# Performance work log

Measured on AMD Instinct MI355X. Metric: run time of the kernel, lower is better.

## Reference

```python
import jax, jax.numpy as jnp
import numpy as np

N_CLASSES = 2  # FS-MOL binary labels


def setup_inputs() -> dict:
    key = jax.random.key(0)
    k1, k2, k3 = jax.random.split(key, 3)
    Ns, Nq, d = 512, 16384, 512
    support_features = jax.random.normal(k1, (Ns, d), dtype=jnp.float32)
    support_labels = jax.random.randint(k2, (Ns,), 0, N_CLASSES, dtype=jnp.int64)
    query_features = jax.random.normal(k3, (Nq, d), dtype=jnp.float32)
    return {
        "support_features": support_features,
        "support_labels": support_labels,
        "query_features": query_features,
    }


def _cov(x):
    # rowvar=False covariance of [N, d] -> [d, d], matching _estimate_cov
    xc = x - jnp.mean(x, axis=0, keepdims=True)
    return (xc.T @ xc) / (x.shape[0] - 1)


def reference(support_features, support_labels, query_features):
    d = support_features.shape[1]
    dt = support_features.dtype
    task_cov = _cov(support_features)          # [d, d]
    reg = jnp.asarray(0.1, dt) * jnp.eye(d, dtype=dt)

    def per_class(c):
        mask = (support_labels == c).astype(dt)            # [Ns]
        n = mask.sum()                                      # scalar count
        mean = (mask[:, None] * support_features).sum(0) / n
        xc = (support_features - mean) * mask[:, None]      # zero out other classes
        cov_c = (xc.T @ xc) / (n - 1.0)
        lam = jnp.minimum(n / (n + 1.0), jnp.asarray(0.1, dt))
        prec = jnp.linalg.inv(lam * cov_c + (1.0 - lam) * task_cov + reg)
        return mean, prec

    means, precs = jax.vmap(per_class)(jnp.arange(N_CLASSES))  # [C,d], [C,d,d]

    # Mahalanobis: diff[c,q,:] = mean_c - query_q  (matches repeated_class_means - repeated_target)
    diff = means[:, None, :] - query_features[None, :, :]      # [C, Nq, d]
    h = jnp.einsum('cqd,cde->cqe', diff, precs)                # [C, Nq, d]
    logits = -(h * diff).sum(-1).T                             # [Nq, C]
    return logits
```

## Files before the change

### kernel.cpp

```cpp
#include <hip/hip_runtime.h>

#define NS 512
#define DF 512
#define NQ 16384

#define WS_MEAN0 0
#define WS_MEAN1 512
#define WS_MEANA 1024
#define WS_CNT   1536
#define WS_V0    2048
#define WS_V1    2560
#define WS_KC    3072
#define WS_M     4096
#define WS_PB    (WS_M + 2*DF*DF)
#define WS_QB    (WS_PB + DF*DF)
#define WS_GP    WS_QB
#define WS_UC    WS_PB
#define WS_VC    (WS_PB + 2*2*8*4096)

typedef __attribute__((ext_vector_type(8))) short short8;
typedef __attribute__((ext_vector_type(4))) float floatx4;

__device__ __forceinline__ unsigned short f2bf(float f) {
    unsigned u = __float_as_uint(f);
    unsigned r = (u + 0x7fffu + ((u >> 16) & 1u)) >> 16;
    return (unsigned short)r;
}

__device__ __forceinline__ float readlane_f(float v, int lane) {
    return __uint_as_float(__builtin_amdgcn_readlane(__float_as_uint(v), lane));
}

__device__ __forceinline__ void load_lds16(const void* g, void* l) {
    __builtin_amdgcn_global_load_lds(
        (const __attribute__((address_space(1))) unsigned int*)g,
        (__attribute__((address_space(3))) unsigned int*)l, 16, 0, 0);
}

__device__ __forceinline__ void gj_invert64(float* T, float (*rbuf)[4][64], int tid) {
    int jl = tid & 63, w = tid >> 6;
    float Tr[16];
#pragma unroll
    for (int m = 0; m < 16; ++m) Tr[m] = T[(w * 16 + m) * 66 + jl];
#pragma unroll
    for (int r = 0; r < 16; ++r) {
        const int q0 = r * 4;
        const int par = r & 1;
        if (w == (q0 >> 4)) {
            const int mb = q0 & 15;
            rbuf[par][0][jl] = Tr[mb + 0];
            rbuf[par][1][jl] = Tr[mb + 1];
            rbuf[par][2][jl] = Tr[mb + 2];
            rbuf[par][3][jl] = Tr[mb + 3];
        }
        __syncthreads();
        float B[4][4];
#pragma unroll
        for (int a = 0; a < 4; ++a)
#pragma unroll
            for (int bb = 0; bb < 4; ++bb) B[a][bb] = rbuf[par][a][q0 + bb];
#pragma unroll
        for (int p = 0; p < 4; ++p) {
            float piv = 1.0f / B[p][p];
#pragma unroll
            for (int j = 0; j < 4; ++j) if (j != p) B[p][j] *= piv;
#pragma unroll
            for (int i = 0; i < 4; ++i) if (i != p) {
                float f = B[i][p];
#pragma unroll
                for (int j = 0; j < 4; ++j) if (j != p) B[i][j] -= f * B[p][j];
                B[i][p] = -f * piv;
            }
            B[p][p] = piv;
        }
        float r0v = rbuf[par][0][jl], r1v = rbuf[par][1][jl];
        float r2v = rbuf[par][2][jl], r3v = rbuf[par][3][jl];
        float nr[4];
#pragma unroll
        for (int a = 0; a < 4; ++a)
            nr[a] = B[a][0] * r0v + B[a][1] * r1v + B[a][2] * r2v + B[a][3] * r3v;
        bool colin = ((jl >> 2) == r);
        int bsel = jl & 3;
        float Bc[4];
#pragma unroll
        for (int a = 0; a < 4; ++a)
            Bc[a] = bsel == 0 ? B[a][0]
                  : (bsel == 1 ? B[a][1] : (bsel == 2 ? B[a][2] : B[a][3]));
#pragma unroll
        for (int m = 0; m < 16; ++m) {
            float cv0 = readlane_f(Tr[m], q0 + 0);
            float cv1 = readlane_f(Tr[m], q0 + 1);
            float cv2 = readlane_f(Tr[m], q0 + 2);
            float cv3 = readlane_f(Tr[m], q0 + 3);
            float g = Tr[m] - (cv0 * nr[0] + cv1 * nr[1] + cv2 * nr[2] + cv3 * nr[3]);
            bool rowin = (((w * 16 + m) >> 2) == r);
            float gcol = -(cv0 * Bc[0] + cv1 * Bc[1] + cv2 * Bc[2] + cv3 * Bc[3]);
            if (rowin) g = nr[m & 3];
            if (colin) g = rowin ? Bc[m & 3] : gcol;
            Tr[m] = g;
        }
    }
#pragma unroll
    for (int m = 0; m < 16; ++m) T[(w * 16 + m) * 66 + jl] = Tr[m];
    __syncthreads();
}

__global__ __launch_bounds__(256) void k_front(const float* __restrict__ S,
                                               const int* __restrict__ lab,
                                               float* __restrict__ ws) {
    int b = blockIdx.x, tid = threadIdx.x;
    if (b >= 512) {
        __shared__ int slb[NS];
        __shared__ float r0[4][64], r1[4][64];
        __shared__ int rc[4];
        int bs = b - 512;
        for (int l = tid; l < NS; l += 256) slb[l] = lab[l];
        __syncthreads();
        int dl = tid & 63, ch = tid >> 6;
        int dd = bs * 64 + dl;
        float s0 = 0.f, s1 = 0.f;
        int n1 = 0;
        for (int n = ch * 128; n < ch * 128 + 128; ++n) {
            float v = S[n * DF + dd];
            if (slb[n]) { s1 += v; n1++; } else { s0 += v; }
        }
        r0[ch][dl] = s0; r1[ch][dl] = s1;
        if (dl == 0) rc[ch] = n1;
        __syncthreads();
        if (ch == 0) {
            float t0 = 0.f, t1 = 0.f; int n1t = 0;
#pragma unroll
            for (int x = 0; x < 4; ++x) { t0 += r0[x][dl]; t1 += r1[x][dl]; n1t += rc[x]; }
            float fn1 = (float)n1t, fn0 = (float)(NS - n1t);
            ws[WS_MEAN0 + dd] = t0 / fn0;
            ws[WS_MEAN1 + dd] = t1 / fn1;
            ws[WS_MEANA + dd] = (t0 + t1) / (float)NS;
            if (bs == 0 && dl == 0) {
                ws[WS_CNT] = fn0; ws[WS_CNT + 1] = fn1;
                ws[WS_KC] = 0.f; ws[WS_KC + 1] = 0.f;
            }
        }
        return;
    }
    __shared__ float SA[16 * 65];
    __shared__ float SB[16 * 65];
    __shared__ int lb[16];
    int tx = tid & 15, ty = tid >> 4;
    int i0 = (b & 7) * 64, j0 = ((b >> 3) & 7) * 64;
    int z = b >> 6;
    float a0[4][4] = {{0.f}}, a1[4][4] = {{0.f}};
    for (int nc = z * 64; nc < z * 64 + 64; nc += 16) {
#pragma unroll
        for (int l = 0; l < 4; ++l) {
            int idx = tid + 256 * l;
            int nn = idx >> 6, col = idx & 63;
            SA[nn * 65 + col] = S[(nc + nn) * DF + i0 + col];
            SB[nn * 65 + col] = S[(nc + nn) * DF + j0 + col];
        }
        if (tid < 16) lb[tid] = lab[nc + tid];
        __syncthreads();
#pragma unroll
        for (int kk = 0; kk < 16; ++kk) {
            float av[4], bv[4];
#pragma unroll
            for (int r = 0; r < 4; ++r) av[r] = SA[kk * 65 + ty * 4 + r];
#pragma unroll
            for (int s = 0; s < 4; ++s) bv[s] = SB[kk * 65 + tx * 4 + s];
            if (lb[kk]) {
#pragma unroll
                for (int r = 0; r < 4; ++r)
#pragma unroll
                    for (int s = 0; s < 4; ++s) a1[r][s] += av[r] * bv[s];
            } else {
#pragma unroll
                for (int r = 0; r < 4; ++r)
#pragma unroll
                    for (int s = 0; s < 4; ++s) a0[r][s] += av[r] * bv[s];
            }
        }
        __syncthreads();
    }
    float* Gp = ws + WS_GP;
#pragma unroll
    for (int r = 0; r < 4; ++r) {
        int i = i0 + ty * 4 + r;
#pragma unroll
        for (int s = 0; s < 4; ++s) {
            int j = j0 + tx * 4 + s;
            Gp[((z * 2 + 0) * DF + i) * DF + j] = a0[r][s];
            Gp[((z * 2 + 1) * DF + i) * DF + j] = a1[r][s];
        }
    }
}

__global__ __launch_bounds__(256) void k_asm(float* __restrict__ ws) {
    int b = blockIdx.x, tid = threadIdx.x;
    int tx = tid & 15, ty = tid >> 4;
    __shared__ float T[64 * 66];
    __shared__ float rbuf[2][4][64];
    const float* Gp = ws + WS_GP;
    float n0 = ws[WS_CNT], n1 = ws[WS_CNT + 1];
    float lam0 = fminf(n0 / (n0 + 1.f), 0.1f);
    float lam1 = fminf(n1 / (n1 + 1.f), 0.1f);
    bool dup = (b == 64);
    int ti = dup ? 0 : (b >> 3), tj = dup ? 0 : (b & 7);
    int jb = tj * 64 + tx * 4;
    float4 m0j = *(const float4*)&ws[WS_MEAN0 + jb];
    float4 m1j = *(const float4*)&ws[WS_MEAN1 + jb];
    float4 maj = *(const float4*)&ws[WS_MEANA + jb];
    float out0[4][4], out1[4][4];
#pragma unroll
    for (int r = 0; r < 4; ++r) {
        int i = ti * 64 + ty * 4 + r;
        float m0i = ws[WS_MEAN0 + i], m1i = ws[WS_MEAN1 + i], mai = ws[WS_MEANA + i];
        float4 g0 = make_float4(0.f, 0.f, 0.f, 0.f);
        float4 g1 = make_float4(0.f, 0.f, 0.f, 0.f);
#pragma unroll
        for (int ch = 0; ch < 8; ++ch) {
            float4 a = *(const float4*)&Gp[((ch * 2 + 0) * DF + i) * DF + jb];
            float4 bb = *(const float4*)&Gp[((ch * 2 + 1) * DF + i) * DF + jb];
            g0.x += a.x; g0.y += a.y; g0.z += a.z; g0.w += a.w;
            g1.x += bb.x; g1.y += bb.y; g1.z += bb.z; g1.w += bb.w;
        }
        float g0a[4] = {g0.x, g0.y, g0.z, g0.w};
        float g1a[4] = {g1.x, g1.y, g1.z, g1.w};
        float m0ja[4] = {m0j.x, m0j.y, m0j.z, m0j.w};
        float m1ja[4] = {m1j.x, m1j.y, m1j.z, m1j.w};
        float maja[4] = {maj.x, maj.y, maj.z, maj.w};
#pragma unroll
        for (int s = 0; s < 4; ++s) {
            int j = jb + s;
            float task = (g0a[s] + g1a[s] - (float)NS * mai * maja[s]) / (float)(NS - 1);
            float cov0 = (g0a[s] - n0 * m0i * m0ja[s]) / (n0 - 1.f);
            float cov1 = (g1a[s] - n1 * m1i * m1ja[s]) / (n1 - 1.f);
            float dg = (i == j) ? 0.1f : 0.f;
            out0[r][s] = lam0 * cov0 + (1.f - lam0) * task + dg;
            out1[r][s] = lam1 * cov1 + (1.f - lam1) * task + dg;
        }
    }
    if (!dup) {
#pragma unroll
        for (int r = 0; r < 4; ++r) {
            int i = ti * 64 + ty * 4 + r;
            *(float4*)&ws[WS_M + (size_t)i * DF + jb] = make_float4(out0[r][0], out0[r][1], out0[r][2], out0[r][3]);
            *(float4*)&ws[WS_M + DF * DF + (size_t)i * DF + jb] = make_float4(out1[r][0], out1[r][1], out1[r][2], out1[r][3]);
        }
        if (ti == 0 && tj != 0) {
            float* u0 = ws + WS_UC + ((0 * 2 + 0) * 8 + tj) * 4096;
            float* u1 = ws + WS_UC + ((0 * 2 + 1) * 8 + tj) * 4096;
#pragma unroll
            for (int r = 0; r < 4; ++r) {
                int il = ty * 4 + r, jl = tx * 4;
                *(float4*)&u0[il * 64 + jl] = make_float4(out0[r][0], out0[r][1], out0[r][2], out0[r][3]);
                *(float4*)&u1[il * 64 + jl] = make_float4(out1[r][0], out1[r][1], out1[r][2], out1[r][3]);
            }
        }
        if (tj == 0 && ti != 0) {
            float* v0 = ws + WS_VC + ((0 * 2 + 0) * 8 + ti) * 4096;
            float* v1 = ws + WS_VC + ((0 * 2 + 1) * 8 + ti) * 4096;
#pragma unroll
            for (int r = 0; r < 4; ++r) {
                int il = ty * 4 + r, jl = tx * 4;
                *(float4*)&v0[il * 64 + jl] = make_float4(out0[r][0], out0[r][1], out0[r][2], out0[r][3]);
                *(float4*)&v1[il * 64 + jl] = make_float4(out1[r][0], out1[r][1], out1[r][2], out1[r][3]);
            }
        }
    }
    if (b == 0 || dup) {
#pragma unroll
        for (int r = 0; r < 4; ++r)
#pragma unroll
            for (int s = 0; s < 4; ++s)
                T[(ty * 4 + r) * 66 + tx * 4 + s] = dup ? out1[r][s] : out0[r][s];
        __syncthreads();
        gj_invert64(T, rbuf, tid);
        float* scr = ws + WS_UC + ((0 * 2 + (dup ? 1 : 0)) * 8 + 0) * 4096;
#pragma unroll
        for (int m = 0; m < 16; ++m) {
            int idx = tid + 256 * m;
            int i = idx >> 6, j = idx & 63;
            scr[i * 64 + j] = T[i * 66 + j];
        }
    }
}

__global__ __launch_bounds__(256) void k_fgj(float* __restrict__ ws, int k) {
    int c = blockIdx.y, jh = blockIdx.z;
    int x = blockIdx.x;
    int ti = x >> 3, tj = x & 7;
    int par = k & 1, npar = par ^ 1;
    int tid = threadIdx.x;
    int cb0 = jh * 32;
    float* Mb = ws + WS_M + (size_t)c * DF * DF;
    const float* UCi = ws + WS_UC + (par * 2 + c) * 8 * 4096;
    const float* VCi = ws + WS_VC + (par * 2 + c) * 8 * 4096;
    float* UCo = ws + WS_UC + (npar * 2 + c) * 8 * 4096;
    float* VCo = ws + WS_VC + (npar * 2 + c) * 8 * 4096;
    const float* scr_in = UCi + k * 4096;

    if (ti == k && tj == k) {
        float* Akk = Mb + (k * 64) * DF + k * 64;
#pragma unroll
        for (int m = 0; m < 8; ++m) {
            int idx = tid + 256 * m;
            int i = idx >> 5, j = idx & 31;
            Akk[i * DF + cb0 + j] = scr_in[i * 64 + cb0 + j];
        }
        return;
    }
    bool isrow = (ti == k);
    bool iscol = (tj == k);
    bool spec = (ti == k + 1) && (tj == k + 1);
    if ((iscol || spec) && jh == 1) return;

    __shared__ float T[64 * 68];
    __shared__ float V[64 * 66];
    __shared__ float U[64 * 68];
    __shared__ float D[64 * 68];
    __shared__ float rbuf[2][4][64];

#pragma unroll
    for (int m = 0; m < 16; ++m) {
        int idx = tid + 256 * m;
        int i = idx >> 6, j = idx & 63;
        T[i * 68 + j] = scr_in[i * 64 + j];
    }

    if (isrow) {
        const float* uc = UCi + tj * 4096;
#pragma unroll
        for (int m = 0; m < 8; ++m) {
            int idx = tid + 256 * m;
            int i = idx >> 5, j = idx & 31;
            U[i * 68 + j] = uc[i * 64 + cb0 + j];
        }
        __syncthreads();
        int tx8 = tid & 7, ty32 = tid >> 3;
        float acc[2][4] = {{0.f}};
#pragma unroll 8
        for (int kk = 0; kk < 64; ++kk) {
            float a0 = T[(ty32 * 2 + 0) * 68 + kk];
            float a1 = T[(ty32 * 2 + 1) * 68 + kk];
            float4 bv = *(const float4*)&U[kk * 68 + tx8 * 4];
            acc[0][0] += a0 * bv.x; acc[0][1] += a0 * bv.y; acc[0][2] += a0 * bv.z; acc[0][3] += a0 * bv.w;
            acc[1][0] += a1 * bv.x; acc[1][1] += a1 * bv.y; acc[1][2] += a1 * bv.z; acc[1][3] += a1 * bv.w;
        }
        float* dst = Mb + (k * 64) * DF + tj * 64 + cb0;
#pragma unroll
        for (int r = 0; r < 2; ++r) {
            int row = ty32 * 2 + r;
            float4 o = make_float4(acc[r][0], acc[r][1], acc[r][2], acc[r][3]);
            *(float4*)&dst[row * DF + tx8 * 4] = o;
            if (tj == k + 1)
                *(float4*)&VCo[k * 4096 + row * 64 + cb0 + tx8 * 4] = o;
        }
        return;
    }

    if (iscol) {
        const float* vc = VCi + ti * 4096;
#pragma unroll
        for (int m = 0; m < 16; ++m) {
            int idx = tid + 256 * m;
            int i = idx >> 6, j = idx & 63;
            V[i * 66 + j] = vc[i * 64 + j];
        }
        __syncthreads();
        int tx16 = tid & 15, ty16 = tid >> 4;
        float acc[4][4] = {{0.f}};
#pragma unroll 8
        for (int kk = 0; kk < 64; ++kk) {
            float a[4];
#pragma unroll
            for (int r = 0; r < 4; ++r) a[r] = V[(ty16 * 4 + r) * 66 + kk];
            float4 bv = *(const float4*)&T[kk * 68 + tx16 * 4];
#pragma unroll
            for (int r = 0; r < 4; ++r) {
                acc[r][0] += a[r] * bv.x; acc[r][1] += a[r] * bv.y;
                acc[r][2] += a[r] * bv.z; acc[r][3] += a[r] * bv.w;
            }
        }
        float* dst = Mb + (ti * 64) * DF + k * 64;
#pragma unroll
        for (int r = 0; r < 4; ++r) {
            int row = ty16 * 4 + r;
            float4 o = make_float4(-acc[r][0], -acc[r][1], -acc[r][2], -acc[r][3]);
            *(float4*)&dst[row * DF + tx16 * 4] = o;
            if (ti == k + 1)
                *(float4*)&UCo[k * 4096 + row * 64 + tx16 * 4] = o;
        }
        return;
    }

    if (!spec) {
        const float* vc = VCi + ti * 4096;
#pragma unroll
        for (int m = 0; m < 16; ++m) {
            int idx = tid + 256 * m;
            int i = idx >> 6, j = idx & 63;
            V[i * 66 + j] = vc[i * 64 + j];
        }
        const float* uc = UCi + tj * 4096;
#pragma unroll
        for (int m = 0; m < 8; ++m) {
            int idx = tid + 256 * m;
            int i = idx >> 5, j = idx & 31;
            U[i * 68 + j] = uc[i * 64 + cb0 + j];
        }
        __syncthreads();
        int tx8 = tid & 7, ty32 = tid >> 3;
        float a1[2][4] = {{0.f}};
#pragma unroll 8
        for (int kk = 0; kk < 64; ++kk) {
            float v0 = T[(ty32 * 2 + 0) * 68 + kk];
            float v1 = T[(ty32 * 2 + 1) * 68 + kk];
            float4 bv = *(const float4*)&U[kk * 68 + tx8 * 4];
            a1[0][0] += v0 * bv.x; a1[0][1] += v0 * bv.y; a1[0][2] += v0 * bv.z; a1[0][3] += v0 * bv.w;
            a1[1][0] += v1 * bv.x; a1[1][1] += v1 * bv.y; a1[1][2] += v1 * bv.z; a1[1][3] += v1 * bv.w;
        }
#pragma unroll
        for (int r = 0; r < 2; ++r)
            *(float4*)&D[(ty32 * 2 + r) * 68 + tx8 * 4] = make_float4(a1[r][0], a1[r][1], a1[r][2], a1[r][3]);
        __syncthreads();
        float a2[2][4] = {{0.f}};
#pragma unroll 8
        for (int kk = 0; kk < 64; ++kk) {
            float v0 = V[(ty32 * 2 + 0) * 66 + kk];
            float v1 = V[(ty32 * 2 + 1) * 66 + kk];
            float4 bv = *(const float4*)&D[kk * 68 + tx8 * 4];
            a2[0][0] += v0 * bv.x; a2[0][1] += v0 * bv.y; a2[0][2] += v0 * bv.z; a2[0][3] += v0 * bv.w;
            a2[1][0] += v1 * bv.x; a2[1][1] += v1 * bv.y; a2[1][2] += v1 * bv.z; a2[1][3] += v1 * bv.w;
        }
        float* dst = Mb + (ti * 64) * DF + tj * 64 + cb0;
#pragma unroll
        for (int r = 0; r < 2; ++r) {
            int row = ty32 * 2 + r;
            float4 old = *(const float4*)&dst[row * DF + tx8 * 4];
            float4 nv = make_float4(old.x - a2[r][0], old.y - a2[r][1], old.z - a2[r][2], old.w - a2[r][3]);
            *(float4*)&dst[row * DF + tx8 * 4] = nv;
            if (tj == k + 1)
                *(float4*)&VCo[ti * 4096 + row * 64 + cb0 + tx8 * 4] = nv;
            if (ti == k + 1)
                *(float4*)&UCo[tj * 4096 + row * 64 + cb0 + tx8 * 4] = nv;
        }
        return;
    }

    {
        const float* vc = VCi + (k + 1) * 4096;
#pragma unroll
        for (int m = 0; m < 16; ++m) {
            int idx = tid + 256 * m;
            int i = idx >> 6, j = idx & 63;
            V[i * 66 + j] = vc[i * 64 + j];
        }
        const float* uc = UCi + (k + 1) * 4096;
#pragma unroll
        for (int m = 0; m < 16; ++m) {
            int idx = tid + 256 * m;
            int i = idx >> 6, j = idx & 63;
            U[i * 68 + j] = uc[i * 64 + j];
        }
        __syncthreads();
        int tx16 = tid & 15, ty16 = tid >> 4;
        float d[4][4] = {{0.f}};
#pragma unroll 8
        for (int kk = 0; kk < 64; ++kk) {
            float a[4];
#pragma unroll
            for (int r = 0; r < 4; ++r) a[r] = T[(ty16 * 4 + r) * 68 + kk];
            float4 bv = *(const float4*)&U[kk * 68 + tx16 * 4];
#pragma unroll
            for (int r = 0; r < 4; ++r) {
                d[r][0] += a[r] * bv.x; d[r][1] += a[r] * bv.y;
                d[r][2] += a[r] * bv.z; d[r][3] += a[r] * bv.w;
            }
        }
#pragma unroll
        for (int r = 0; r < 4; ++r)
            *(float4*)&D[(ty16 * 4 + r) * 68 + tx16 * 4] = make_float4(d[r][0], d[r][1], d[r][2], d[r][3]);
        __syncthreads();
        float y[4][4] = {{0.f}};
#pragma unroll 8
        for (int kk = 0; kk < 64; ++kk) {
            float a[4];
#pragma unroll
            for (int r = 0; r < 4; ++r) a[r] = V[(ty16 * 4 + r) * 66 + kk];
            float4 bv = *(const float4*)&D[kk * 68 + tx16 * 4];
#pragma unroll
            for (int r = 0; r < 4; ++r) {
                y[r][0] += a[r] * bv.x; y[r][1] += a[r] * bv.y;
                y[r][2] += a[r] * bv.z; y[r][3] += a[r] * bv.w;
            }
        }
        const float* dst = Mb + (size_t)((k + 1) * 64) * DF + (k + 1) * 64;
        float4 nv[4];
#pragma unroll
        for (int r = 0; r < 4; ++r) {
            int row = ty16 * 4 + r;
            float4 old = *(const float4*)&dst[row * DF + tx16 * 4];
            nv[r] = make_float4(old.x - y[r][0], old.y - y[r][1], old.z - y[r][2], old.w - y[r][3]);
        }
        __syncthreads();
#pragma unroll
        for (int r = 0; r < 4; ++r) {
            int row = ty16 * 4 + r;
            V[row * 66 + tx16 * 4 + 0] = nv[r].x;
            V[row * 66 + tx16 * 4 + 1] = nv[r].y;
            V[row * 66 + tx16 * 4 + 2] = nv[r].z;
            V[row * 66 + tx16 * 4 + 3] = nv[r].w;
        }
        __syncthreads();
        gj_invert64(V, rbuf, tid);
        float* so = UCo + (k + 1) * 4096;
#pragma unroll
        for (int m = 0; m < 16; ++m) {
            int idx = tid + 256 * m;
            int i = idx >> 6, j = idx & 63;
            so[i * 64 + j] = V[i * 66 + j];
        }
    }
}

__global__ __launch_bounds__(256) void k_vkbf(float* __restrict__ ws) {
    int b = blockIdx.x;
    int tid = threadIdx.x;
    if (b >= 16) {
        int e = (b - 16) * 2048 + tid * 8;
        const float* M = ws + WS_M;
        unsigned short* pbw = (unsigned short*)(ws + WS_PB);
        float4 x0 = *(const float4*)&M[e];
        float4 x1 = *(const float4*)&M[e + 4];
        short8 r;
        r[0] = (short)f2bf(x0.x); r[1] = (short)f2bf(x0.y);
        r[2] = (short)f2bf(x0.z); r[3] = (short)f2bf(x0.w);
        r[4] = (short)f2bf(x1.x); r[5] = (short)f2bf(x1.y);
        r[6] = (short)f2bf(x1.z); r[7] = (short)f2bf(x1.w);
        *(short8*)(pbw + e) = r;
        return;
    }
    int c = b >> 3, rb = b & 7;
    const float* P = ws + WS_M + (size_t)c * DF * DF;
    const float* mc = ws + (c ? WS_MEAN1 : WS_MEAN0);
    float* v = ws + (c ? WS_V1 : WS_V0);
    __shared__ float ml[DF];
    __shared__ float red[4][64];
    for (int l = tid; l < DF; l += 256) ml[l] = mc[l];
    __syncthreads();
    int rl = tid & 63, ch = tid >> 6;
    int row = rb * 64 + rl;
    float dot = 0.f;
    const float* pr = P + (size_t)row * DF + ch * 128;
    for (int t = 0; t < 32; ++t) {
        float4 pv = *(const float4*)(pr + t * 4);
        const float* mm = ml + ch * 128 + t * 4;
        dot += pv.x * mm[0] + pv.y * mm[1] + pv.z * mm[2] + pv.w * mm[3];
    }
    red[ch][rl] = dot;
    __syncthreads();
    if (ch == 0) {
        float d = red[0][rl] + red[1][rl] + red[2][rl] + red[3][rl];
        v[row] = d;
        float kp = d * ml[row];
#pragma unroll
        for (int off = 32; off > 0; off >>= 1) kp += __shfl_down(kp, off);
        if (rl == 0) atomicAdd(&ws[WS_KC + c], kp);
    }
}

__global__ __launch_bounds__(256) void k_qinit(const float* __restrict__ Q,
                                               float* __restrict__ ws,
                                               float* __restrict__ out) {
    unsigned short* qbw = (unsigned short*)(ws + WS_QB);
    const float* v0 = ws + WS_V0;
    const float* v1 = ws + WS_V1;
    int lane = threadIdx.x & 63;
    int q = blockIdx.x * 4 + (threadIdx.x >> 6);
    const float* qrow = Q + (size_t)q * DF + lane * 8;
    float4 x0 = *(const float4*)(qrow);
    float4 x1 = *(const float4*)(qrow + 4);
    const float* v0p = v0 + lane * 8;
    const float* v1p = v1 + lane * 8;
    float4 w00 = *(const float4*)(v0p), w01 = *(const float4*)(v0p + 4);
    float4 w10 = *(const float4*)(v1p), w11 = *(const float4*)(v1p + 4);
    float a0 = x0.x * w00.x + x0.y * w00.y + x0.z * w00.z + x0.w * w00.w
             + x1.x * w01.x + x1.y * w01.y + x1.z * w01.z + x1.w * w01.w;
    float a1 = x0.x * w10.x + x0.y * w10.y + x0.z * w10.z + x0.w * w10.w
             + x1.x * w11.x + x1.y * w11.y + x1.z * w11.z + x1.w * w11.w;
    short8 r;
    r[0] = (short)f2bf(x0.x); r[1] = (short)f2bf(x0.y);
    r[2] = (short)f2bf(x0.z); r[3] = (short)f2bf(x0.w);
    r[4] = (short)f2bf(x1.x); r[5] = (short)f2bf(x1.y);
    r[6] = (short)f2bf(x1.z); r[7] = (short)f2bf(x1.w);
    *(short8*)(qbw + (size_t)q * DF + lane * 8) = r;
#pragma unroll
    for (int off = 32; off > 0; off >>= 1) {
        a0 += __shfl_down(a0, off);
        a1 += __shfl_down(a1, off);
    }
    if (lane == 0) {
        out[q * 2 + 0] = 2.f * a0 - ws[WS_KC + 0];
        out[q * 2 + 1] = 2.f * a1 - ws[WS_KC + 1];
    }
}

__global__ __launch_bounds__(256, 3) void k_gemm(const float* __restrict__ ws,
                                                 float* __restrict__ out) {
    const unsigned short* qb = (const unsigned short*)(ws + WS_QB);
    int c = blockIdx.y >> 2;
    int n0 = (blockIdx.y & 3) * 128;
    const unsigned short* pbc = (const unsigned short*)(ws + WS_PB) + (size_t)c * DF * DF;
    int q0 = blockIdx.x * 128;
    __shared__ __align__(16) unsigned short Abuf[128 * 64];
    __shared__ __align__(16) unsigned short Bbuf[128 * 64];
    int tid = threadIdx.x;
    int w = tid >> 6, lane = tid & 63;
    int quad = lane >> 4, l15 = lane & 15;
    floatx4 acc[2][8];
#pragma unroll
    for (int mt = 0; mt < 2; ++mt)
#pragma unroll
        for (int nt = 0; nt < 8; ++nt) acc[mt][nt] = (floatx4)(0.f);

    for (int kt = 0; kt < 8; ++kt) {
        int kc2 = kt * 64;
#pragma unroll
        for (int i = 0; i < 4; ++i) {
            int o = tid * 16 + i * 4096;
            int row = o >> 7;
            int sg = ((o >> 4) & 7) ^ (row & 7);
            load_lds16(qb + (size_t)(q0 + row) * DF + kc2 + sg * 8, (char*)Abuf + o);
        }
#pragma unroll
        for (int i = 0; i < 4; ++i) {
            int o = tid * 16 + i * 4096;
            int row = o >> 7;
            int sg = ((o >> 4) & 7) ^ (row & 7);
            load_lds16(pbc + (size_t)(n0 + row) * DF + kc2 + sg * 8, (char*)Bbuf + o);
        }
        __syncthreads();
#pragma unroll
        for (int kk2 = 0; kk2 < 2; ++kk2) {
            int u = ((kk2 * 4 + quad) ^ (l15 & 7)) << 4;
            short8 b[8];
#pragma unroll
            for (int nt = 0; nt < 8; ++nt)
                b[nt] = *(const short8*)((const char*)Bbuf + (nt * 16 + l15) * 128 + u);
#pragma unroll
            for (int mt = 0; mt < 2; ++mt) {
                short8 a = *(const short8*)((const char*)Abuf + (w * 32 + mt * 16 + l15) * 128 + u);
#pragma unroll
                for (int nt = 0; nt < 8; ++nt)
                    acc[mt][nt] = __builtin_amdgcn_mfma_f32_16x16x32_bf16(a, b[nt], acc[mt][nt], 0, 0, 0);
            }
        }
        __syncthreads();
    }
#pragma unroll
    for (int mt = 0; mt < 2; ++mt)
#pragma unroll
        for (int reg = 0; reg < 4; ++reg) {
            int row = w * 32 + mt * 16 + quad * 4 + reg;
            float part = 0.f;
#pragma unroll
            for (int nt = 0; nt < 8; ++nt) {
                float h = acc[mt][nt][reg];
                unsigned qu = qb[(size_t)(q0 + row) * DF + n0 + nt * 16 + l15];
                part += h * __uint_as_float(qu << 16);
            }
            part += __shfl_xor(part, 1);
            part += __shfl_xor(part, 2);
            part += __shfl_xor(part, 4);
            part += __shfl_xor(part, 8);
            if (l15 == 0) atomicAdd(&out[(size_t)(q0 + row) * 2 + c], -part);
        }
}

extern "C" void kernel_launch(void* const* d_in, const int* in_sizes, int n_in,
                              void* d_out, int out_size, void* d_ws, size_t ws_size,
                              hipStream_t stream) {
    const float* S = (const float*)d_in[0];
    const int* lab = (const int*)d_in[1];
    const float* Q = (const float*)d_in[2];
    float* out = (float*)d_out;
    float* ws = (float*)d_ws;

    k_front<<<520, 256, 0, stream>>>(S, lab, ws);
    k_asm<<<65, 256, 0, stream>>>(ws);
    for (int k = 0; k < 8; ++k)
        k_fgj<<<dim3(64, 2, 2), 256, 0, stream>>>(ws, k);
    k_vkbf<<<272, 256, 0, stream>>>(ws);
    k_qinit<<<NQ / 4, 256, 0, stream>>>(Q, ws, out);
    k_gemm<<<dim3(NQ / 128, 8), 256, 0, stream>>>(ws, out);
}
```

Baseline: 342.0 us.

## Overlap query bf16 conversion with the latency-bound block Gauss-Jordan launches

Adds extra blocks to each of the eight k_fgj launches that convert a slice of the query matrix from fp32 to bf16 into the workspace, filling otherwise idle GPU capacity. k_qinit then reads the bf16 copy instead of fp32 Q, so the later kernel does less memory traffic. The linear term now uses bf16-rounded queries, which slightly changes numerics. It also relies on the GP scratch that aliases the QB region not being used after these writes.

```diff
diff --git a/kernel.cpp b/kernel.cpp
--- a/kernel.cpp
+++ b/kernel.cpp
@@ -25,6 +25,10 @@
     unsigned u = __float_as_uint(f);
     unsigned r = (u + 0x7fffu + ((u >> 16) & 1u)) >> 16;
     return (unsigned short)r;
+}
+
+__device__ __forceinline__ float bf2f(unsigned short u) {
+    return __uint_as_float(((unsigned)u) << 16);
 }
 
 __device__ __forceinline__ float readlane_f(float v, int lane) {
@@ -284,12 +288,28 @@
     }
 }
 
-__global__ __launch_bounds__(256) void k_fgj(float* __restrict__ ws, int k) {
+__global__ __launch_bounds__(256) void k_fgj(const float* __restrict__ Q,
+                                             float* __restrict__ ws, int k) {
     int c = blockIdx.y, jh = blockIdx.z;
     int x = blockIdx.x;
+    int tid = threadIdx.x;
+
+    if (x >= 64) {
+        int cb = (x - 64) + 128 * (c + 2 * jh);
+        size_t e = (size_t)k * 1048576 + (size_t)cb * 2048 + tid * 8;
+        float4 x0 = *(const float4*)(Q + e);
+        float4 x1 = *(const float4*)(Q + e + 4);
+        short8 r;
+        r[0] = (short)f2bf(x0.x); r[1] = (short)f2bf(x0.y);
+        r[2] = (short)f2bf(x0.z); r[3] = (short)f2bf(x0.w);
+        r[4] = (short)f2bf(x1.x); r[5] = (short)f2bf(x1.y);
+        r[6] = (short)f2bf(x1.z); r[7] = (short)f2bf(x1.w);
+        *(short8*)((unsigned short*)(ws + WS_QB) + e) = r;
+        return;
+    }
+
     int ti = x >> 3, tj = x & 7;
     int par = k & 1, npar = par ^ 1;
-    int tid = threadIdx.x;
     int cb0 = jh * 32;
     float* Mb = ws + WS_M + (size_t)c * DF * DF;
     const float* UCi = ws + WS_UC + (par * 2 + c) * 8 * 4096;
@@ -568,31 +588,25 @@
     }
 }
 
-__global__ __launch_bounds__(256) void k_qinit(const float* __restrict__ Q,
-                                               float* __restrict__ ws,
+__global__ __launch_bounds__(256) void k_qinit(float* __restrict__ ws,
                                                float* __restrict__ out) {
-    unsigned short* qbw = (unsigned short*)(ws + WS_QB);
+    const unsigned short* qbw = (const unsigned short*)(ws + WS_QB);
     const float* v0 = ws + WS_V0;
     const float* v1 = ws + WS_V1;
     int lane = threadIdx.x & 63;
     int q = blockIdx.x * 4 + (threadIdx.x >> 6);
-    const float* qrow = Q + (size_t)q * DF + lane * 8;
-    float4 x0 = *(const float4*)(qrow);
-    float4 x1 = *(const float4*)(qrow + 4);
+    short8 qv = *(const short8*)(qbw + (size_t)q * DF + lane * 8);
+    float xx[8];
+#pragma unroll
+    for (int j = 0; j < 8; ++j) xx[j] = bf2f((unsigned short)qv[j]);
     const float* v0p = v0 + lane * 8;
     const float* v1p = v1 + lane * 8;
     float4 w00 = *(const float4*)(v0p), w01 = *(const float4*)(v0p + 4);
     float4 w10 = *(const float4*)(v1p), w11 = *(const float4*)(v1p + 4);
-    float a0 = x0.x * w00.x + x0.y * w00.y + x0.z * w00.z + x0.w * w00.w
-             + x1.x * w01.x + x1.y * w01.y + x1.z * w01.z + x1.w * w01.w;
-    float a1 = x0.x * w10.x + x0.y * w10.y + x0.z * w10.z + x0.w * w10.w
-             + x1.x * w11.x + x1.y * w11.y + x1.z * w11.z + x1.w * w11.w;
-    short8 r;
-    r[0] = (short)f2bf(x0.x); r[1] = (short)f2bf(x0.y);
-    r[2] = (short)f2bf(x0.z); r[3] = (short)f2bf(x0.w);
-    r[4] = (short)f2bf(x1.x); r[5] = (short)f2bf(x1.y);
-    r[6] = (short)f2bf(x1.z); r[7] = (short)f2bf(x1.w);
-    *(short8*)(qbw + (size_t)q * DF + lane * 8) = r;
+    float a0 = xx[0] * w00.x + xx[1] * w00.y + xx[2] * w00.z + xx[3] * w00.w
+             + xx[4] * w01.x + xx[5] * w01.y + xx[6] * w01.z + xx[7] * w01.w;
+    float a1 = xx[0] * w10.x + xx[1] * w10.y + xx[2] * w10.z + xx[3] * w10.w
+             + xx[4] * w11.x + xx[5] * w11.y + xx[6] * w11.z + xx[7] * w11.w;
 #pragma unroll
     for (int off = 32; off > 0; off >>= 1) {
         a0 += __shfl_down(a0, off);
@@ -688,8 +702,8 @@
     k_front<<<520, 256, 0, stream>>>(S, lab, ws);
     k_asm<<<65, 256, 0, stream>>>(ws);
     for (int k = 0; k < 8; ++k)
-        k_fgj<<<dim3(64, 2, 2), 256, 0, stream>>>(ws, k);
+        k_fgj<<<dim3(192, 2, 2), 256, 0, stream>>>(Q, ws, k);
     k_vkbf<<<272, 256, 0, stream>>>(ws);
-    k_qinit<<<NQ / 4, 256, 0, stream>>>(Q, ws, out);
+    k_qinit<<<NQ / 4, 256, 0, stream>>>(ws, out);
     k_gemm<<<dim3(NQ / 128, 8), 256, 0, stream>>>(ws, out);
 }
```

New measurement: 342.7 us. About the same (+0.2%).
